# Kernel tuning notes

Measured on AMD Instinct MI355X. Metric: run time of the kernel, lower is better.

## Reference

```python
import jax, jax.numpy as jnp
import numpy as np

N, K, D_IN, D_OUT = 50000, 32, 128, 128
TEMPERATURE = 1.0


def setup_inputs() -> dict:
    key = jax.random.key(0)
    k1, k2, k3 = jax.random.split(key, 3)
    feat = jax.random.normal(k1, (N, D_IN), dtype=jnp.float32)
    # Glorot-like scale so pairwise distances stay in a reasonable softmax range
    weight = jax.random.normal(k2, (D_IN, D_OUT), dtype=jnp.float32) / np.sqrt(D_IN)
    bias = jnp.zeros((D_OUT,), dtype=jnp.float32)
    # norm='none' -> unit edge weights; fixed-degree-k graph -> topk returns all k neighbors
    top_k_weights = jnp.ones((N, K), dtype=jnp.float32)
    top_k_idx = jax.random.randint(k3, (N, K), 0, N, dtype=jnp.int64)
    return {"feat": feat, "weight": weight, "bias": bias,
            "top_k_weights": top_k_weights, "top_k_idx": top_k_idx}


def reference(feat, weight, bias, top_k_weights, top_k_idx):
    # Linear projection (self.weight): [n, d_out]
    h = feat @ weight
    # Gather top-k neighbor embeddings: [n, k, d]
    fk = h[top_k_idx]
    mask = top_k_idx == -1                      # [n, k] missing-neighbor mask
    w = jnp.where(mask, 0.0, top_k_weights)     # zero out missing weights

    # Pairwise Euclidean distances among each node's k neighbors: [n, k, k]
    # ||a-b|| = sqrt(|a|^2 + |b|^2 - 2 a.b); avoids materializing [n,k,k,d]
    sq = jnp.sum(fk * fk, axis=-1)                          # [n, k]
    gram = jnp.einsum('nkd,nmd->nkm', fk, fk)               # [n, k, k]
    d2 = sq[:, :, None] + sq[:, None, :] - 2.0 * gram
    d2 = jnp.maximum(d2, 0.0)
    dist = jnp.sqrt(jnp.where(d2 > 0.0, d2, 1.0))
    dist = jnp.where(d2 > 0.0, dist, 0.0)                   # zero for identical pts / -1 idx
    # zero entries for missing pairs (matches partial_distance_matrix semantics)
    pair_mask = mask[:, :, None] | mask[:, None, :]
    dist = jnp.where(pair_mask, 0.0, dist)

    # Weighted sum of distances over neighbors (medoid cost): [n, k]
    dagg = jnp.einsum('nm,nkm->nk', w, dist)
    big = jnp.finfo(dist.dtype).max
    dagg = jnp.where(mask | ~jnp.isfinite(dagg), big, dagg)

    # Soft medoid weights
    r = jax.nn.softmax(-dagg / TEMPERATURE, axis=-1)
    # with_weight_correction=True
    r = r * w
    r = r / jnp.sum(r, axis=-1, keepdims=True)
    r = jnp.where(mask, 0.0, r)

    # spmm over the reliable adjacency: [n, d_out]
    out = jnp.einsum('nk,nkd->nd', r, fk)
    return out + bias
```

## Files before the change

### kernel.cpp

```cpp
#include <hip/hip_runtime.h>
#include <math.h>


typedef __attribute__((ext_vector_type(2)))  _Float16 half2v;
typedef __attribute__((ext_vector_type(4)))  _Float16 half4v;
typedef __attribute__((ext_vector_type(8)))  _Float16 half8;
typedef __attribute__((ext_vector_type(16))) float    f32x16;

#define NK   32
#define DIM  128
#define ROWB 272
#define WPB  3

__global__ __launch_bounds__(256) void prep(const float* __restrict__ W,
                                            _Float16* __restrict__ WT) {
    int t  = blockIdx.x * 256 + threadIdx.x;
    int nn = t >> 7, k = t & 127;
    WT[t] = (_Float16)W[k * 128 + nn];
}

__global__ __launch_bounds__(64) void gemm128(
    const float* __restrict__ A, const _Float16* __restrict__ WT,
    _Float16* __restrict__ Hq, int n)
{
    const int lane = threadIdx.x;
    const int l31  = lane & 31;
    const int hf   = lane >> 5;

    const int row  = blockIdx.x * 32 + l31;
    const int rowc = row < n ? row : n - 1;

    f32x16 acc[4];
#pragma unroll
    for (int t = 0; t < 4; ++t)
#pragma unroll
        for (int i = 0; i < 16; ++i) acc[t][i] = 0.0f;

    const float* ap = A + (size_t)rowc * 128 + 8 * hf;
#pragma unroll
    for (int s = 0; s < 8; ++s) {
        float4 b0 = *reinterpret_cast<const float4*>(ap + 16 * s);
        float4 b1 = *reinterpret_cast<const float4*>(ap + 16 * s + 4);
        half8 bf;
        bf[0] = (_Float16)b0.x; bf[1] = (_Float16)b0.y;
        bf[2] = (_Float16)b0.z; bf[3] = (_Float16)b0.w;
        bf[4] = (_Float16)b1.x; bf[5] = (_Float16)b1.y;
        bf[6] = (_Float16)b1.z; bf[7] = (_Float16)b1.w;
#pragma unroll
        for (int t = 0; t < 4; ++t) {
            half8 af = *reinterpret_cast<const half8*>(
                WT + (size_t)(l31 + 32 * t) * 128 + 16 * s + 8 * hf);
            acc[t] = __builtin_amdgcn_mfma_f32_32x32x16_f16(af, bf, acc[t], 0, 0, 0);
        }
    }

    if (row < n) {
        _Float16* hp = Hq + (size_t)row * 128;
#pragma unroll
        for (int t = 0; t < 4; ++t)
#pragma unroll
            for (int g = 0; g < 4; ++g) {
                half4v hv;
#pragma unroll
                for (int q = 0; q < 4; ++q) hv[q] = (_Float16)acc[t][4 * g + q];
                *reinterpret_cast<half4v*>(hp + 32 * t + 8 * g + 4 * hf) = hv;
            }
    }
}

__global__ __launch_bounds__(192, 4) void softk(
    const _Float16* __restrict__ hq, const float* __restrict__ bias,
    const float* __restrict__ tkw, const int* __restrict__ idx,
    float* __restrict__ out, int n)
{
    __shared__ __align__(16) char  fkT[WPB][NK * ROWB];
    __shared__ __align__(16) float rbuf[WPB][NK];

    const int w    = threadIdx.x >> 6;
    const int lane = threadIdx.x & 63;
    const int l31  = lane & 31;
    const int hf   = lane >> 5;
    const int g    = lane >> 4;
    const int m    = lane & 15;
    const int pbase = (lane & 32) + ((lane & 32) >> 3);

    char* fkw = &fkT[w][0];

    const int d0 = 2 * lane;
    const float2 bv = *reinterpret_cast<const float2*>(bias + d0);
    const float4* rb = reinterpret_cast<const float4*>(&rbuf[w][0]);
    const int wbase = ROWB * g + 16 * ((m + 4 * g) & 15);
    const int fbase = ROWB * l31;
    const int uc0   = 4 * hf + 16 * (l31 & 3);
    int eaddr[4];
#pragma unroll
    for (int p = 0; p < 4; ++p) eaddr[p] = 4 * ((lane + 16 * p) & 63);

    const int stride = gridDim.x * WPB;
    int nd = blockIdx.x * WPB + w;
    if (nd >= n) return;

    int   vid = idx[(size_t)nd * NK + l31];
    float tw  = tkw[(size_t)nd * NK + l31];
    int   mkc = (vid < 0) ? 1 : 0;
    float wc  = mkc ? 0.0f : tw;
    half8 gb[8];
    {
        int idr = mkc ? 0 : vid;
#pragma unroll
        for (int i = 0; i < 8; ++i) {
            int idg = __shfl(idr, 4 * i + g, 64);
            gb[i] = *reinterpret_cast<const half8*>(
                hq + (size_t)idg * DIM + 8 * m);
        }
    }

    while (true) {
        const int  ndn = nd + stride;
        const bool hn  = ndn < n;

        int vid_n = 0; float tw_n = 0.0f;
        if (hn) {
            vid_n = idx[(size_t)ndn * NK + l31];
            tw_n  = tkw[(size_t)ndn * NK + l31];
        }

#pragma unroll
        for (int i = 0; i < 8; ++i)
            *reinterpret_cast<half8*>(&fkw[1088 * i + wbase]) = gb[i];

        f32x16 acc;
#pragma unroll
        for (int i = 0; i < 16; ++i) acc[i] = 0.0f;
        float sqp = 0.0f;
        int u = uc0;
#pragma unroll
        for (int s = 0; s < 8; ++s) {
            half8 fr = *reinterpret_cast<const half8*>(&fkw[fbase + 4 * (u & 63)]);
            u += 8;
            acc = __builtin_amdgcn_mfma_f32_32x32x16_f16(fr, fr, acc, 0, 0, 0);
            const half2v* p2 = reinterpret_cast<const half2v*>(&fr);
#pragma unroll
            for (int q = 0; q < 4; ++q)
                sqp = __builtin_amdgcn_fdot2(p2[q], p2[q], sqp, false);
        }
        float sq = sqp + __shfl_xor(sqp, 32, 64);

        const int mk_n = (vid_n < 0) ? 1 : 0;
        half8 gb_n[8];
        if (hn) {
            int idr_n = mk_n ? 0 : vid_n;
#pragma unroll
            for (int i = 0; i < 8; ++i) {
                int idg = __shfl(idr_n, 4 * i + g, 64);
                gb_n[i] = *reinterpret_cast<const half8*>(
                    hq + (size_t)idg * DIM + 8 * m);
            }
        }

        {
            _Float16 shi = (_Float16)sq;
            _Float16 slo = (_Float16)(sq - (float)shi);
            _Float16 nh  = (_Float16)(-0.5f * (float)shi);
            _Float16 nl  = (_Float16)(-0.5f * (float)slo);
            _Float16 z   = (_Float16)0.0f, one = (_Float16)1.0f;
            half8 aext = {z, z, z, z, z, z, z, z};
            half8 bext = {z, z, z, z, z, z, z, z};
            if (hf == 0) {
                aext[0] = nh;  aext[1] = nl;  aext[2] = one; aext[3] = one;
                bext[0] = one; bext[1] = one; bext[2] = nh;  bext[3] = nl;
            }
            acc = __builtin_amdgcn_mfma_f32_32x32x16_f16(aext, bext, acc, 0, 0, 0);
        }

        float pt[4] = {0.0f, 0.0f, 0.0f, 0.0f};
#pragma unroll
        for (int reg = 0; reg < 16; ++reg) {
            const int c = (reg & 3) + 8 * (reg >> 2);
            float wr = __shfl(wc, pbase + c, 64);
            float d2 = fmaxf(-(acc[reg] + acc[reg]), 0.0f);
            float ds = (d2 > 1e-4f) ? __builtin_amdgcn_sqrtf(d2) : 0.0f;
            pt[reg & 3] = fmaf(wr, ds, pt[reg & 3]);
        }
        float part = (pt[0] + pt[1]) + (pt[2] + pt[3]);
        float sA = part + __shfl_xor(part, 32, 64);
        if (mkc || !(sA < 3.4028235e38f)) sA = 3.4028235e38f;

        float x  = -sA;
        float mx = x;
#pragma unroll
        for (int o = 16; o > 0; o >>= 1) mx = fmaxf(mx, __shfl_xor(mx, o, 32));
        float t  = __expf(x - mx) * wc;
        float st = t;
#pragma unroll
        for (int o = 16; o > 0; o >>= 1) st += __shfl_xor(st, o, 32);
        float r = t * __builtin_amdgcn_rcpf(st);

        rbuf[w][l31] = r;

        float o0 = 0.0f, o1 = 0.0f;
#pragma unroll
        for (int q = 0; q < 8; ++q) {
            float4 rv = rb[q];
            half2v h0 = *reinterpret_cast<const half2v*>(&fkw[ROWB * (4 * q + 0) + eaddr[0]]);
            half2v h1 = *reinterpret_cast<const half2v*>(&fkw[ROWB * (4 * q + 1) + eaddr[1]]);
            half2v h2 = *reinterpret_cast<const half2v*>(&fkw[ROWB * (4 * q + 2) + eaddr[2]]);
            half2v h3 = *reinterpret_cast<const half2v*>(&fkw[ROWB * (4 * q + 3) + eaddr[3]]);
            o0 = fmaf(rv.x, (float)h0[0], o0); o1 = fmaf(rv.x, (float)h0[1], o1);
            o0 = fmaf(rv.y, (float)h1[0], o0); o1 = fmaf(rv.y, (float)h1[1], o1);
            o0 = fmaf(rv.z, (float)h2[0], o0); o1 = fmaf(rv.z, (float)h2[1], o1);
            o0 = fmaf(rv.w, (float)h3[0], o0); o1 = fmaf(rv.w, (float)h3[1], o1);
        }
        float2 ov = { o0 + bv.x, o1 + bv.y };
        *reinterpret_cast<float2*>(out + (size_t)nd * DIM + d0) = ov;

        if (!hn) break;
        nd  = ndn;
        mkc = mk_n;
        wc  = mk_n ? 0.0f : tw_n;
#pragma unroll
        for (int i = 0; i < 8; ++i) gb[i] = gb_n[i];
    }
}

extern "C" void kernel_launch(void* const* d_in, const int* in_sizes, int n_in,
                              void* d_out, int out_size, void* d_ws, size_t ws_size,
                              hipStream_t stream) {
    const float* feat = (const float*)d_in[0];
    const float* W    = (const float*)d_in[1];
    const float* bias = (const float*)d_in[2];
    const float* tkw  = (const float*)d_in[3];
    const int*   idx  = (const int*)d_in[4];
    float* out = (float*)d_out;

    const int n = in_sizes[0] / DIM;
    _Float16* hq = (_Float16*)d_ws;
    _Float16* wt = hq + (size_t)n * DIM;

    const int gblocks = (n + 31) / 32;
    const int sblocks = (n + 4 * WPB - 1) / (4 * WPB);

    prep<<<64, 256, 0, stream>>>(W, wt);
    gemm128<<<gblocks, 64, 0, stream>>>(feat, wt, hq, n);
    softk<<<sblocks, 192, 0, stream>>>(hq, bias, tkw, idx, out, n);
}
```

Baseline: 155.6 us.

## Fuse prep, GEMM and soft-medoid kernels into one cooperative persistent kernel

Merges the weight-transpose, projection GEMM and soft-medoid aggregation into a single cooperative kernel that uses grid-wide syncs between phases, with a grid sized from the occupancy query. The aim is to remove two kernel launches and the gaps between them. The original three-kernel path is kept as a fallback if the cooperative launch fails. In exchange the GEMM phase now runs with 3 waves per 192-thread block over a fixed persistent grid instead of many small 64-thread blocks, and the grid barriers add their own sync cost.

Measured after the change: 319.4 us. +105.3%, slower.

```diff
diff --git a/kernel.cpp b/kernel.cpp
--- a/kernel.cpp
+++ b/kernel.cpp
@@ -1,5 +1,8 @@
 #include <hip/hip_runtime.h>
+#include <hip/hip_cooperative_groups.h>
 #include <math.h>
+
+namespace cg = cooperative_groups;
 
 
 typedef __attribute__((ext_vector_type(2)))  _Float16 half2v;
@@ -11,6 +14,224 @@
 #define DIM  128
 #define ROWB 272
 #define WPB  3
+
+__global__ __launch_bounds__(192, 4) void fused(
+    const float* __restrict__ feat, const float* __restrict__ W,
+    const float* __restrict__ bias, const float* __restrict__ tkw,
+    const int* __restrict__ idx, float* __restrict__ out,
+    _Float16* __restrict__ hq, _Float16* __restrict__ wt, int n)
+{
+    cg::grid_group gg = cg::this_grid();
+
+    __shared__ __align__(16) char  fkT[WPB][NK * ROWB];
+    __shared__ __align__(16) float rbuf[WPB][NK];
+
+    const int w    = threadIdx.x >> 6;
+    const int lane = threadIdx.x & 63;
+    const int l31  = lane & 31;
+    const int hf   = lane >> 5;
+
+    {
+        int t0 = blockIdx.x * 192 + threadIdx.x;
+        if (t0 < DIM * DIM) {
+            int nn = t0 >> 7, k = t0 & 127;
+            wt[t0] = (_Float16)W[k * 128 + nn];
+        }
+    }
+    gg.sync();
+
+    {
+        const int nwaves = gridDim.x * WPB;
+        const int gw     = blockIdx.x * WPB + w;
+        const int ntiles = (n + 31) >> 5;
+        for (int tile = gw; tile < ntiles; tile += nwaves) {
+            const int row  = tile * 32 + l31;
+            const int rowc = row < n ? row : n - 1;
+
+            f32x16 gacc[4];
+#pragma unroll
+            for (int t = 0; t < 4; ++t)
+#pragma unroll
+                for (int i = 0; i < 16; ++i) gacc[t][i] = 0.0f;
+
+            const float* ap = feat + (size_t)rowc * 128 + 8 * hf;
+#pragma unroll
+            for (int s = 0; s < 8; ++s) {
+                float4 b0 = *reinterpret_cast<const float4*>(ap + 16 * s);
+                float4 b1 = *reinterpret_cast<const float4*>(ap + 16 * s + 4);
+                half8 bf;
+                bf[0] = (_Float16)b0.x; bf[1] = (_Float16)b0.y;
+                bf[2] = (_Float16)b0.z; bf[3] = (_Float16)b0.w;
+                bf[4] = (_Float16)b1.x; bf[5] = (_Float16)b1.y;
+                bf[6] = (_Float16)b1.z; bf[7] = (_Float16)b1.w;
+#pragma unroll
+                for (int t = 0; t < 4; ++t) {
+                    half8 af = *reinterpret_cast<const half8*>(
+                        wt + (size_t)(l31 + 32 * t) * 128 + 16 * s + 8 * hf);
+                    gacc[t] = __builtin_amdgcn_mfma_f32_32x32x16_f16(af, bf, gacc[t], 0, 0, 0);
+                }
+            }
+
+            if (row < n) {
+                _Float16* hp = hq + (size_t)row * 128;
+#pragma unroll
+                for (int t = 0; t < 4; ++t)
+#pragma unroll
+                    for (int gq = 0; gq < 4; ++gq) {
+                        half4v hv;
+#pragma unroll
+                        for (int q = 0; q < 4; ++q) hv[q] = (_Float16)gacc[t][4 * gq + q];
+                        *reinterpret_cast<half4v*>(hp + 32 * t + 8 * gq + 4 * hf) = hv;
+                    }
+            }
+        }
+    }
+    gg.sync();
+
+    {
+        const int g    = lane >> 4;
+        const int m    = lane & 15;
+        const int pbase = (lane & 32) + ((lane & 32) >> 3);
+
+        char* fkw = &fkT[w][0];
+
+        const int d0 = 2 * lane;
+        const float2 bv = *reinterpret_cast<const float2*>(bias + d0);
+        const float4* rb = reinterpret_cast<const float4*>(&rbuf[w][0]);
+        const int wbase = ROWB * g + 16 * ((m + 4 * g) & 15);
+        const int fbase = ROWB * l31;
+        const int uc0   = 4 * hf + 16 * (l31 & 3);
+        int eaddr[4];
+#pragma unroll
+        for (int p = 0; p < 4; ++p) eaddr[p] = 4 * ((lane + 16 * p) & 63);
+
+        const int stride = gridDim.x * WPB;
+        int nd = blockIdx.x * WPB + w;
+        if (nd >= n) return;
+
+        int   vid = idx[(size_t)nd * NK + l31];
+        float tw  = tkw[(size_t)nd * NK + l31];
+        int   mkc = (vid < 0) ? 1 : 0;
+        float wc  = mkc ? 0.0f : tw;
+        half8 gb[8];
+        {
+            int idr = mkc ? 0 : vid;
+#pragma unroll
+            for (int i = 0; i < 8; ++i) {
+                int idg = __shfl(idr, 4 * i + g, 64);
+                gb[i] = *reinterpret_cast<const half8*>(
+                    hq + (size_t)idg * DIM + 8 * m);
+            }
+        }
+
+        while (true) {
+            const int  ndn = nd + stride;
+            const bool hn  = ndn < n;
+
+            int vid_n = 0; float tw_n = 0.0f;
+            if (hn) {
+                vid_n = idx[(size_t)ndn * NK + l31];
+                tw_n  = tkw[(size_t)ndn * NK + l31];
+            }
+
+#pragma unroll
+            for (int i = 0; i < 8; ++i)
+                *reinterpret_cast<half8*>(&fkw[1088 * i + wbase]) = gb[i];
+
+            f32x16 acc;
+#pragma unroll
+            for (int i = 0; i < 16; ++i) acc[i] = 0.0f;
+            float sqp = 0.0f;
+            int u = uc0;
+#pragma unroll
+            for (int s = 0; s < 8; ++s) {
+                half8 fr = *reinterpret_cast<const half8*>(&fkw[fbase + 4 * (u & 63)]);
+                u += 8;
+                acc = __builtin_amdgcn_mfma_f32_32x32x16_f16(fr, fr, acc, 0, 0, 0);
+                const half2v* p2 = reinterpret_cast<const half2v*>(&fr);
+#pragma unroll
+                for (int q = 0; q < 4; ++q)
+                    sqp = __builtin_amdgcn_fdot2(p2[q], p2[q], sqp, false);
+            }
+            float sq = sqp + __shfl_xor(sqp, 32, 64);
+
+            const int mk_n = (vid_n < 0) ? 1 : 0;
+            half8 gb_n[8];
+            if (hn) {
+                int idr_n = mk_n ? 0 : vid_n;
+#pragma unroll
+                for (int i = 0; i < 8; ++i) {
+                    int idg = __shfl(idr_n, 4 * i + g, 64);
+                    gb_n[i] = *reinterpret_cast<const half8*>(
+                        hq + (size_t)idg * DIM + 8 * m);
+                }
+            }
+
+            {
+                _Float16 shi = (_Float16)sq;
+                _Float16 slo = (_Float16)(sq - (float)shi);
+                _Float16 nh  = (_Float16)(-0.5f * (float)shi);
+                _Float16 nl  = (_Float16)(-0.5f * (float)slo);
+                _Float16 z   = (_Float16)0.0f, one = (_Float16)1.0f;
+                half8 aext = {z, z, z, z, z, z, z, z};
+                half8 bext = {z, z, z, z, z, z, z, z};
+                if (hf == 0) {
+                    aext[0] = nh;  aext[1] = nl;  aext[2] = one; aext[3] = one;
+                    bext[0] = one; bext[1] = one; bext[2] = nh;  bext[3] = nl;
+                }
+                acc = __builtin_amdgcn_mfma_f32_32x32x16_f16(aext, bext, acc, 0, 0, 0);
+            }
+
+            float pt[4] = {0.0f, 0.0f, 0.0f, 0.0f};
+#pragma unroll
+            for (int reg = 0; reg < 16; ++reg) {
+                const int c = (reg & 3) + 8 * (reg >> 2);
+                float wr = __shfl(wc, pbase + c, 64);
+                float d2 = fmaxf(-(acc[reg] + acc[reg]), 0.0f);
+                float ds = (d2 > 1e-4f) ? __builtin_amdgcn_sqrtf(d2) : 0.0f;
+                pt[reg & 3] = fmaf(wr, ds, pt[reg & 3]);
+            }
+            float part = (pt[0] + pt[1]) + (pt[2] + pt[3]);
+            float sA = part + __shfl_xor(part, 32, 64);
+            if (mkc || !(sA < 3.4028235e38f)) sA = 3.4028235e38f;
+
+            float x  = -sA;
+            float mx = x;
+#pragma unroll
+            for (int o = 16; o > 0; o >>= 1) mx = fmaxf(mx, __shfl_xor(mx, o, 32));
+            float tt = __expf(x - mx) * wc;
+            float st = tt;
+#pragma unroll
+            for (int o = 16; o > 0; o >>= 1) st += __shfl_xor(st, o, 32);
+            float r = tt * __builtin_amdgcn_rcpf(st);
+
+            rbuf[w][l31] = r;
+
+            float o0 = 0.0f, o1 = 0.0f;
+#pragma unroll
+            for (int q = 0; q < 8; ++q) {
+                float4 rv = rb[q];
+                half2v h0 = *reinterpret_cast<const half2v*>(&fkw[ROWB * (4 * q + 0) + eaddr[0]]);
+                half2v h1 = *reinterpret_cast<const half2v*>(&fkw[ROWB * (4 * q + 1) + eaddr[1]]);
+                half2v h2 = *reinterpret_cast<const half2v*>(&fkw[ROWB * (4 * q + 2) + eaddr[2]]);
+                half2v h3 = *reinterpret_cast<const half2v*>(&fkw[ROWB * (4 * q + 3) + eaddr[3]]);
+                o0 = fmaf(rv.x, (float)h0[0], o0); o1 = fmaf(rv.x, (float)h0[1], o1);
+                o0 = fmaf(rv.y, (float)h1[0], o0); o1 = fmaf(rv.y, (float)h1[1], o1);
+                o0 = fmaf(rv.z, (float)h2[0], o0); o1 = fmaf(rv.z, (float)h2[1], o1);
+                o0 = fmaf(rv.w, (float)h3[0], o0); o1 = fmaf(rv.w, (float)h3[1], o1);
+            }
+            float2 ov = { o0 + bv.x, o1 + bv.y };
+            *reinterpret_cast<float2*>(out + (size_t)nd * DIM + d0) = ov;
+
+            if (!hn) break;
+            nd  = ndn;
+            mkc = mk_n;
+            wc  = mk_n ? 0.0f : tw_n;
+#pragma unroll
+            for (int i = 0; i < 8; ++i) gb[i] = gb_n[i];
+        }
+    }
+}
 
 __global__ __launch_bounds__(256) void prep(const float* __restrict__ W,
                                             _Float16* __restrict__ WT) {
@@ -237,10 +458,32 @@
     _Float16* hq = (_Float16*)d_ws;
     _Float16* wt = hq + (size_t)n * DIM;
 
-    const int gblocks = (n + 31) / 32;
-    const int sblocks = (n + 4 * WPB - 1) / (4 * WPB);
-
-    prep<<<64, 256, 0, stream>>>(W, wt);
-    gemm128<<<gblocks, 64, 0, stream>>>(feat, wt, hq, n);
-    softk<<<sblocks, 192, 0, stream>>>(hq, bias, tkw, idx, out, n);
+    static int bpc = 0;
+    if (bpc == 0) {
+        int v = 0;
+        hipError_t e = hipOccupancyMaxActiveBlocksPerMultiprocessor(&v, fused, 192, 0);
+        bpc = (e == hipSuccess && v >= 1) ? v : -1;
+        if (bpc > 8) bpc = 8;
+    }
+
+    bool done = false;
+    if (bpc > 0) {
+        int grid = bpc * 256;
+        int nn = n;
+        void* args[] = { (void*)&feat, (void*)&W, (void*)&bias, (void*)&tkw,
+                         (void*)&idx, (void*)&out, (void*)&hq, (void*)&wt,
+                         (void*)&nn };
+        hipError_t e = hipLaunchCooperativeKernel(fused, dim3(grid), dim3(192),
+                                                  args, 0, stream);
+        if (e == hipSuccess) done = true;
+        else bpc = -1;
+    }
+
+    if (!done) {
+        const int gblocks = (n + 31) / 32;
+        const int sblocks = (n + 4 * WPB - 1) / (4 * WPB);
+        prep<<<64, 256, 0, stream>>>(W, wt);
+        gemm128<<<gblocks, 64, 0, stream>>>(feat, wt, hq, n);
+        softk<<<sblocks, 192, 0, stream>>>(hq, bias, tkw, idx, out, n);
+    }
 }
```
